# Kernel optimization log

Hardware: AMD Instinct MI355X
Metric: run time of the kernel (lower is better)

The kernel has to match this reference:

```python
import jax, jax.numpy as jnp
import numpy as np

B, S, HID = 4, 2048, 2048
NH, NKV, HD = 16, 4, 128
GROUPS = NH // NKV
THETA = 10000.0
SCALING = 1.0
SCALE = HD ** -0.5


def setup_inputs() -> dict:
    key = jax.random.key(0)
    k1, k2, k3 = jax.random.split(key, 3)
    hidden_states = jax.random.normal(k1, (B, S, HID), dtype=jnp.float32)
    # stored as [in, out] so x @ W matches torch Linear(x) with W = weight.T
    W_qkv = jax.random.normal(k2, (HID, (NH + 2 * NKV) * HD), dtype=jnp.float32) * (HID ** -0.5)
    W_o = jax.random.normal(k3, (HID, HID), dtype=jnp.float32) * (HID ** -0.5)
    return {"hidden_states": hidden_states, "W_qkv": W_qkv, "W_o": W_o}


def _rope_tables(seq_len, dtype):
    inv_freq = 1.0 / (THETA ** (jnp.arange(0, HD, 2, dtype=jnp.float32) / HD))
    t = jnp.arange(seq_len, dtype=jnp.float32) / SCALING
    freqs = jnp.einsum("s,d->sd", t, inv_freq)          # [S, HD/2]
    emb = jnp.concatenate([freqs, freqs], axis=-1)        # [S, HD]
    return jnp.cos(emb).astype(dtype), jnp.sin(emb).astype(dtype)


def _rotate_half(x):
    x1, x2 = jnp.split(x, 2, axis=-1)
    return jnp.concatenate([-x2, x1], axis=-1)


def _apply_rope(x, cos, sin):
    # x: [B, H, S, D]; cos/sin: [S, D]
    return x * cos[None, None] + _rotate_half(x) * sin[None, None]


def reference(hidden_states, W_qkv, W_o):
    b, s, _ = hidden_states.shape
    qkv = hidden_states @ W_qkv                           # [B, S, (NH+2NKV)*HD]
    q, k, v = jnp.split(qkv, [NH * HD, (NH + NKV) * HD], axis=-1)
    q = q.reshape(b, s, NH, HD).transpose(0, 2, 1, 3)      # [B, NH, S, D]
    k = k.reshape(b, s, NKV, HD).transpose(0, 2, 1, 3)     # [B, NKV, S, D]
    v = v.reshape(b, s, NKV, HD).transpose(0, 2, 1, 3)

    cos, sin = _rope_tables(s, hidden_states.dtype)
    q = _apply_rope(q, cos, sin)
    k = _apply_rope(k, cos, sin)

    # GQA attention without materializing expanded K/V
    qg = q.reshape(b, NKV, GROUPS, s, HD)                  # [B, NKV, G, Sq, D]
    scores = jnp.einsum("bkgqd,bkKd->bkgqK", qg, k) * SCALE
    causal = jnp.tril(jnp.ones((s, s), dtype=bool))
    scores = jnp.where(causal[None, None, None], scores, jnp.finfo(scores.dtype).min)
    probs = jax.nn.softmax(scores, axis=-1)
    out = jnp.einsum("bkgqK,bkKd->bkgqd", probs, v)        # [B, NKV, G, Sq, D]
    out = out.reshape(b, NH, s, HD).transpose(0, 2, 1, 3).reshape(b, s, HID)
    return out @ W_o
```

## Files before the change

kernel.cpp:

```cpp
#include <hip/hip_runtime.h>

#define B_ 4
#define S_ 2048
#define HID_ 2048
#define NH_ 16
#define NKV_ 4
#define HD_ 128
#define NTOK (B_ * S_)
#define QKV_N 3072
#define KO_N 512
#define SCALE_ 0.08838834764831845f
#define QSC_ 0.12751743f
#define NEG_ -30000.0f

typedef __attribute__((ext_vector_type(8))) short short8;
typedef __attribute__((ext_vector_type(4))) short short4v;
typedef __attribute__((ext_vector_type(4))) float f32x4;
typedef unsigned short ushort_t;
typedef unsigned int uint32;

__device__ __forceinline__ float sanit(float x) {
    if (!(x == x)) x = 0.0f;
    return fminf(fmaxf(x, -65504.0f), 65504.0f);
}
__device__ __forceinline__ ushort_t f2bf(float f) {
    union { float f; uint32 u; } c; c.f = f;
    uint32 u = c.u;
    u += 0x7fffu + ((u >> 16) & 1u);
    return (ushort_t)(u >> 16);
}
__device__ __forceinline__ ushort_t f2bf_s(float f) { return f2bf(sanit(f)); }
__device__ __forceinline__ float bf2f(ushort_t h) {
    union { float f; uint32 u; } c; c.u = ((uint32)h) << 16;
    return c.f;
}

__device__ __forceinline__ void gl16(const ushort_t* g, ushort_t* l) {
    __builtin_amdgcn_global_load_lds(
        (__attribute__((address_space(1))) void*)g,
        (__attribute__((address_space(3))) void*)l, 16, 0, 0);
}

__global__ void convx_kernel(const float* __restrict__ X, ushort_t* __restrict__ Xb) {
    size_t i = (size_t)blockIdx.x * blockDim.x + threadIdx.x;
    const float4 a = *(const float4*)(X + i * 8);
    const float4 b = *(const float4*)(X + i * 8 + 4);
    short8 p;
    p[0] = (short)f2bf(a.x); p[1] = (short)f2bf(a.y);
    p[2] = (short)f2bf(a.z); p[3] = (short)f2bf(a.w);
    p[4] = (short)f2bf(b.x); p[5] = (short)f2bf(b.y);
    p[6] = (short)f2bf(b.z); p[7] = (short)f2bf(b.w);
    *(short8*)(Xb + i * 8) = p;
}

__global__ void wtrans_kernel(const float* __restrict__ W, ushort_t* __restrict__ Wt,
                              int K, int N) {
    __shared__ float tile[32][33];
    const int n0 = blockIdx.x * 32;
    const int k0 = blockIdx.y * 32;
    const int t  = threadIdx.x;
    const int r  = t >> 3;
    const int c  = (t & 7) * 4;
    const float4 v = *(const float4*)(W + (size_t)(k0 + r) * N + n0 + c);
    tile[r][c] = v.x; tile[r][c + 1] = v.y; tile[r][c + 2] = v.z; tile[r][c + 3] = v.w;
    __syncthreads();
    short4v p;
    p[0] = (short)f2bf(tile[c][r]);
    p[1] = (short)f2bf(tile[c + 1][r]);
    p[2] = (short)f2bf(tile[c + 2][r]);
    p[3] = (short)f2bf(tile[c + 3][r]);
    *(short4v*)(Wt + (size_t)(n0 + r) * K + k0 + c) = p;
}

template <int SPLIT>
__global__ __launch_bounds__(256, 2) void gemm_bt(
    const ushort_t* __restrict__ A, const ushort_t* __restrict__ Bt,
    void* __restrict__ C0, ushort_t* __restrict__ C1, ushort_t* __restrict__ C2,
    int M, int N, int K) {
    __shared__ __align__(16) ushort_t As[128 * 32];
    __shared__ __align__(16) ushort_t Bs[128 * 32];

    const int tid  = threadIdx.x;
    const int lane = tid & 63;
    const int w    = tid >> 6;
    const int wm   = (w >> 1) * 64;
    const int wn   = (w & 1) * 64;
    const int m0   = blockIdx.y * 128;
    const int n0   = blockIdx.x * 128;
    const int col  = lane & 15;
    const int quad = lane >> 4;

    f32x4 acc[4][4] = {};

    const int sr = tid >> 2;
    const int sk = (tid & 3) * 8;
    const ushort_t* ag0 = A + (size_t)(m0 + sr) * K + sk;
    const ushort_t* ag1 = A + (size_t)(m0 + 64 + sr) * K + sk;
    const ushort_t* bg0 = Bt + (size_t)(n0 + sr) * K + sk;
    const ushort_t* bg1 = Bt + (size_t)(n0 + 64 + sr) * K + sk;
    ushort_t* la0 = &As[tid * 8];
    ushort_t* la1 = &As[2048 + tid * 8];
    ushort_t* lb0 = &Bs[tid * 8];
    ushort_t* lb1 = &Bs[2048 + tid * 8];

    for (int k0 = 0; k0 < K; k0 += 32) {
        __syncthreads();
        gl16(ag0 + k0, la0);
        gl16(ag1 + k0, la1);
        gl16(bg0 + k0, lb0);
        gl16(bg1 + k0, lb1);
        __syncthreads();

        short8 af[4], bfr[4];
#pragma unroll
        for (int mt = 0; mt < 4; ++mt)
            af[mt] = *(const short8*)&As[(wm + mt * 16 + col) * 32 + quad * 8];
#pragma unroll
        for (int nt = 0; nt < 4; ++nt)
            bfr[nt] = *(const short8*)&Bs[(wn + nt * 16 + col) * 32 + quad * 8];
#pragma unroll
        for (int mt = 0; mt < 4; ++mt)
#pragma unroll
            for (int nt = 0; nt < 4; ++nt)
                acc[mt][nt] = __builtin_amdgcn_mfma_f32_16x16x32_bf16(
                    af[mt], bfr[nt], acc[mt][nt], 0, 0, 0);
    }

    if (SPLIT) {
        if (n0 >= 2560) {
#pragma unroll
            for (int mt = 0; mt < 4; ++mt)
#pragma unroll
                for (int nt = 0; nt < 4; ++nt) {
                    int cc   = n0 + wn + nt * 16 + col - 2560;
                    int row0 = m0 + wm + mt * 16 + quad * 4;
                    short4v p;
#pragma unroll
                    for (int r = 0; r < 4; ++r) p[r] = (short)f2bf_s(acc[mt][nt][r]);
                    *(short4v*)&C2[(size_t)cc * NTOK + row0] = p;
                }
        } else {
            ushort_t* dst;
            int ldc, coff;
            if (n0 >= 2048) { dst = C1; ldc = KO_N; coff = 2048; }
            else            { dst = (ushort_t*)C0; ldc = HID_; coff = 0; }
#pragma unroll
            for (int mt = 0; mt < 4; ++mt)
#pragma unroll
                for (int nt = 0; nt < 4; ++nt)
#pragma unroll
                    for (int r = 0; r < 4; ++r) {
                        int row = m0 + wm + mt * 16 + quad * 4 + r;
                        int cc  = n0 + wn + nt * 16 + col - coff;
                        dst[(size_t)row * ldc + cc] = f2bf_s(acc[mt][nt][r]);
                    }
        }
    } else {
        float* dst = (float*)C0;
#pragma unroll
        for (int mt = 0; mt < 4; ++mt)
#pragma unroll
            for (int nt = 0; nt < 4; ++nt)
#pragma unroll
                for (int r = 0; r < 4; ++r) {
                    int row = m0 + wm + mt * 16 + quad * 4 + r;
                    int cc  = n0 + wn + nt * 16 + col;
                    dst[(size_t)row * N + cc] = sanit(acc[mt][nt][r]);
                }
    }
}

__global__ void rope_kernel(ushort_t* __restrict__ qbuf,
                            ushort_t* __restrict__ kb) {
    int p = blockIdx.x * blockDim.x + threadIdx.x;
    const int total = NTOK * 20 * 64;
    if (p >= total) return;
    int d    = p & 63;
    int rest = p >> 6;
    int head = rest % 20;
    int tok  = rest / 20;
    int s    = tok & (S_ - 1);

    ushort_t* base;
    float sc;
    if (head < 16) { base = qbuf + (size_t)tok * HID_ + head * HD_ + d; sc = QSC_; }
    else           { base = kb   + (size_t)tok * KO_N + (head - 16) * HD_ + d; sc = 1.0f; }

    float x1 = bf2f(base[0]);
    float x2 = bf2f(base[64]);

    float inv_freq = powf(10000.0f, -(float)d * (1.0f / 64.0f));
    float ang = (float)s * inv_freq;
    float sn, cs;
    sincosf(ang, &sn, &cs);

    base[0]  = f2bf_s((x1 * cs - x2 * sn) * sc);
    base[64] = f2bf_s((x2 * cs + x1 * sn) * sc);
}

__global__ __launch_bounds__(512, 4) void flash_kernel(
    const ushort_t* __restrict__ qbuf, const ushort_t* __restrict__ kb,
    const ushort_t* __restrict__ vtg, ushort_t* __restrict__ obuf) {
    __shared__ __align__(16) ushort_t Ks[64][136];
    __shared__ __align__(16) ushort_t Vt[128][72];
    __shared__ __align__(16) ushort_t Ps[8][16][72];

    const int tid  = threadIdx.x;
    const int lane = tid & 63;
    const int w    = tid >> 6;
    const int col  = lane & 15;
    const int quad = lane >> 4;
    const int q0   = (S_ / 128 - 1 - blockIdx.x) * 128;
    const int h    = blockIdx.y;
    const int b    = blockIdx.z;
    const int kvh  = h >> 2;
    const int bS   = b * S_;

    const int wr    = q0 + w * 16;
    const int wmax  = wr + 15;
    const int i_row = wr + quad * 4;

    short8 qf[4];
    {
        const ushort_t* qp = qbuf + (size_t)(bS + wr + col) * HID_
                             + h * HD_ + quad * 8;
#pragma unroll
        for (int kt = 0; kt < 4; ++kt) qf[kt] = *(const short8*)(qp + kt * 32);
    }

    short8 vone;
#pragma unroll
    for (int e = 0; e < 8; ++e) vone[e] = (short)0x3F80;

    float m_i[4];
#pragma unroll
    for (int r = 0; r < 4; ++r) m_i[r] = NEG_;
    f32x4 o[8] = {};
    f32x4 lsum = {};

    const int ntiles = q0 / 64 + 2;

    const int jr = tid >> 3;
    const int kd = (tid & 7) * 16;
    const int vd = tid >> 2;
    const int vj = (tid & 3) * 16;

    const ushort_t* kgb = kb + (size_t)(bS + jr) * KO_N + kvh * HD_ + kd;
    const ushort_t* vgb = vtg + (size_t)(kvh * HD_ + vd) * NTOK + bS + vj;

    float4 pk0, pk1, pv0, pv1;
    pk0 = *(const float4*)(kgb);
    pk1 = *(const float4*)(kgb + 8);
    pv0 = *(const float4*)(vgb);
    pv1 = *(const float4*)(vgb + 8);
    *(float4*)&Ks[jr][kd]     = pk0;
    *(float4*)&Ks[jr][kd + 8] = pk1;
    *(float4*)&Vt[vd][vj]     = pv0;
    *(float4*)&Vt[vd][vj + 8] = pv1;
    __syncthreads();

    for (int t = 0; t < ntiles; ++t) {
        const int j0 = t * 64;
        const bool pre = (t + 1 < ntiles);
        if (pre) {
            const ushort_t* kgn = kgb + (size_t)(j0 + 64) * KO_N;
            const ushort_t* vgn = vgb + (j0 + 64);
            pk0 = *(const float4*)(kgn);
            pk1 = *(const float4*)(kgn + 8);
            pv0 = *(const float4*)(vgn);
            pv1 = *(const float4*)(vgn + 8);
        }

        if (j0 <= wmax) {
            f32x4 s[4] = {};
#pragma unroll
            for (int ct = 0; ct < 4; ++ct)
#pragma unroll
                for (int kt = 0; kt < 4; ++kt) {
                    short8 kf = *(const short8*)&Ks[ct * 16 + col][kt * 32 + quad * 8];
                    s[ct] = __builtin_amdgcn_mfma_f32_16x16x32_bf16(qf[kt], kf, s[ct], 0, 0, 0);
                }

            if (j0 + 64 > wr) {
#pragma unroll
                for (int ct = 0; ct < 4; ++ct) {
                    int jg = j0 + ct * 16 + col;
#pragma unroll
                    for (int r = 0; r < 4; ++r)
                        if (jg > i_row + r) s[ct][r] = NEG_;
                }
            }

            float mx[4];
#pragma unroll
            for (int r = 0; r < 4; ++r) {
                float m = fmaxf(fmaxf(s[0][r], s[1][r]), fmaxf(s[2][r], s[3][r]));
#pragma unroll
                for (int off = 1; off < 16; off <<= 1)
                    m = fmaxf(m, __shfl_xor(m, off, 64));
                mx[r] = m;
            }
            int ok = 1;
#pragma unroll
            for (int r = 0; r < 4; ++r) ok &= (mx[r] <= m_i[r] + 8.0f) ? 1 : 0;
            if (!__all(ok)) {
#pragma unroll
                for (int r = 0; r < 4; ++r) {
                    float mn = fmaxf(m_i[r], mx[r]);
                    float a  = exp2f(m_i[r] - mn);
                    m_i[r] = mn;
                    lsum[r] *= a;
#pragma unroll
                    for (int dt = 0; dt < 8; ++dt) o[dt][r] *= a;
                }
            }
#pragma unroll
            for (int ct = 0; ct < 4; ++ct)
#pragma unroll
                for (int r = 0; r < 4; ++r)
                    Ps[w][quad * 4 + r][ct * 16 + col] = f2bf(exp2f(s[ct][r] - m_i[r]));

#pragma unroll
            for (int kt = 0; kt < 2; ++kt) {
                short8 pf = *(const short8*)&Ps[w][col][kt * 32 + quad * 8];
#pragma unroll
                for (int dt = 0; dt < 8; ++dt) {
                    short8 vf = *(const short8*)&Vt[dt * 16 + col][kt * 32 + quad * 8];
                    o[dt] = __builtin_amdgcn_mfma_f32_16x16x32_bf16(pf, vf, o[dt], 0, 0, 0);
                }
                lsum = __builtin_amdgcn_mfma_f32_16x16x32_bf16(pf, vone, lsum, 0, 0, 0);
            }
        }

        __syncthreads();
        if (pre) {
            *(float4*)&Ks[jr][kd]     = pk0;
            *(float4*)&Ks[jr][kd + 8] = pk1;
            *(float4*)&Vt[vd][vj]     = pv0;
            *(float4*)&Vt[vd][vj + 8] = pv1;
            __syncthreads();
        }
    }

#pragma unroll
    for (int r = 0; r < 4; ++r) {
        float inv = 1.0f / fmaxf(lsum[r], 1e-30f);
        ushort_t* op = obuf + (size_t)(bS + i_row + r) * HID_ + h * HD_;
#pragma unroll
        for (int dt = 0; dt < 8; ++dt)
            op[dt * 16 + col] = f2bf_s(o[dt][r] * inv);
    }
}

extern "C" void kernel_launch(void* const* d_in, const int* in_sizes, int n_in,
                              void* d_out, int out_size, void* d_ws, size_t ws_size,
                              hipStream_t stream) {
    const float* X    = (const float*)d_in[0];
    const float* Wqkv = (const float*)d_in[1];
    const float* Wo   = (const float*)d_in[2];

    ushort_t* qb  = (ushort_t*)d_out;
    ushort_t* xh  = (ushort_t*)d_out + (size_t)NTOK * HID_;
    ushort_t* kb  = (ushort_t*)d_ws;
    ushort_t* vtg = kb + (size_t)NTOK * KO_N;
    ushort_t* wqt = vtg + (size_t)NTOK * KO_N;
    ushort_t* wot = (ushort_t*)d_ws + (size_t)NTOK * HID_;
    ushort_t* oa  = (ushort_t*)d_ws;

    convx_kernel<<<NTOK * HID_ / (256 * 8), 256, 0, stream>>>(X, xh);
    wtrans_kernel<<<dim3(QKV_N / 32, HID_ / 32), 256, 0, stream>>>(Wqkv, wqt, HID_, QKV_N);
    wtrans_kernel<<<dim3(HID_ / 32, HID_ / 32), 256, 0, stream>>>(Wo, wot, HID_, HID_);
    gemm_bt<1><<<dim3(QKV_N / 128, NTOK / 128), 256, 0, stream>>>(
        xh, wqt, qb, kb, vtg, NTOK, QKV_N, HID_);
    rope_kernel<<<(NTOK * 20 * 64) / 256, 256, 0, stream>>>(qb, kb);
    flash_kernel<<<dim3(S_ / 128, NH_, B_), 512, 0, stream>>>(qb, kb, vtg, xh);
    hipMemcpyAsync(oa, xh, (size_t)NTOK * HID_ * sizeof(ushort_t),
                   hipMemcpyDeviceToDevice, stream);
    gemm_bt<0><<<dim3(HID_ / 128, NTOK / 128), 256, 0, stream>>>(
        oa, wot, d_out, nullptr, nullptr, NTOK, HID_, HID_);
}
```

Baseline: 644.4 us.

## Deepen GEMM K-tile to 64, precompute RoPE tables, vectorize RoPE

The GEMM's K step doubles from 32 to 64, so each shared-memory tile holds twice the data and the number of barrier pairs per block is halved. A new kernel precomputes cos/sin RoPE tables once per call. The RoPE kernel now processes 8 elements per thread with 16-byte loads and reads the tables instead of calling powf/sincosf per element. The trade-off is more LDS per GEMM block, which may reduce occupancy, plus one extra small kernel launch.

```diff
diff --git a/kernel.cpp b/kernel.cpp
--- a/kernel.cpp
+++ b/kernel.cpp
@@ -11,6 +11,7 @@
 #define KO_N 512
 #define SCALE_ 0.08838834764831845f
 #define QSC_ 0.12751743f
+#define LOG2_10K 13.287712379549449f
 #define NEG_ -30000.0f
 
 typedef __attribute__((ext_vector_type(8))) short short8;
@@ -72,13 +73,23 @@
     *(short4v*)(Wt + (size_t)(n0 + r) * K + k0 + c) = p;
 }
 
+__global__ void ropetab_kernel(float* __restrict__ ct, float* __restrict__ st) {
+    int p = blockIdx.x * blockDim.x + threadIdx.x;
+    int s = p >> 6, d = p & 63;
+    float inv = exp2f(-(float)d * (LOG2_10K / 64.0f));
+    float ang = (float)s * inv;
+    float sn, cs;
+    sincosf(ang, &sn, &cs);
+    ct[p] = cs; st[p] = sn;
+}
+
 template <int SPLIT>
 __global__ __launch_bounds__(256, 2) void gemm_bt(
     const ushort_t* __restrict__ A, const ushort_t* __restrict__ Bt,
     void* __restrict__ C0, ushort_t* __restrict__ C1, ushort_t* __restrict__ C2,
     int M, int N, int K) {
-    __shared__ __align__(16) ushort_t As[128 * 32];
-    __shared__ __align__(16) ushort_t Bs[128 * 32];
+    __shared__ __align__(16) ushort_t As[128 * 64];
+    __shared__ __align__(16) ushort_t Bs[128 * 64];
 
     const int tid  = threadIdx.x;
     const int lane = tid & 63;
@@ -92,38 +103,45 @@
 
     f32x4 acc[4][4] = {};
 
-    const int sr = tid >> 2;
-    const int sk = (tid & 3) * 8;
-    const ushort_t* ag0 = A + (size_t)(m0 + sr) * K + sk;
-    const ushort_t* ag1 = A + (size_t)(m0 + 64 + sr) * K + sk;
-    const ushort_t* bg0 = Bt + (size_t)(n0 + sr) * K + sk;
-    const ushort_t* bg1 = Bt + (size_t)(n0 + 64 + sr) * K + sk;
-    ushort_t* la0 = &As[tid * 8];
-    ushort_t* la1 = &As[2048 + tid * 8];
-    ushort_t* lb0 = &Bs[tid * 8];
-    ushort_t* lb1 = &Bs[2048 + tid * 8];
-
-    for (int k0 = 0; k0 < K; k0 += 32) {
+    const ushort_t* agp[4];
+    const ushort_t* bgp[4];
+    ushort_t* lap[4];
+    ushort_t* lbp[4];
+#pragma unroll
+    for (int i = 0; i < 4; ++i) {
+        int c  = i * 256 + tid;
+        int rw = c >> 3;
+        int kc = (c & 7) * 8;
+        agp[i] = A  + (size_t)(m0 + rw) * K + kc;
+        bgp[i] = Bt + (size_t)(n0 + rw) * K + kc;
+        lap[i] = &As[c * 8];
+        lbp[i] = &Bs[c * 8];
+    }
+
+    for (int k0 = 0; k0 < K; k0 += 64) {
         __syncthreads();
-        gl16(ag0 + k0, la0);
-        gl16(ag1 + k0, la1);
-        gl16(bg0 + k0, lb0);
-        gl16(bg1 + k0, lb1);
+#pragma unroll
+        for (int i = 0; i < 4; ++i) gl16(agp[i] + k0, lap[i]);
+#pragma unroll
+        for (int i = 0; i < 4; ++i) gl16(bgp[i] + k0, lbp[i]);
         __syncthreads();
 
-        short8 af[4], bfr[4];
-#pragma unroll
-        for (int mt = 0; mt < 4; ++mt)
-            af[mt] = *(const short8*)&As[(wm + mt * 16 + col) * 32 + quad * 8];
-#pragma unroll
-        for (int nt = 0; nt < 4; ++nt)
-            bfr[nt] = *(const short8*)&Bs[(wn + nt * 16 + col) * 32 + quad * 8];
-#pragma unroll
-        for (int mt = 0; mt < 4; ++mt)
+#pragma unroll
+        for (int kk = 0; kk < 2; ++kk) {
+            short8 af[4], bfr[4];
+#pragma unroll
+            for (int mt = 0; mt < 4; ++mt)
+                af[mt] = *(const short8*)&As[(wm + mt * 16 + col) * 64 + kk * 32 + quad * 8];
 #pragma unroll
             for (int nt = 0; nt < 4; ++nt)
-                acc[mt][nt] = __builtin_amdgcn_mfma_f32_16x16x32_bf16(
-                    af[mt], bfr[nt], acc[mt][nt], 0, 0, 0);
+                bfr[nt] = *(const short8*)&Bs[(wn + nt * 16 + col) * 64 + kk * 32 + quad * 8];
+#pragma unroll
+            for (int mt = 0; mt < 4; ++mt)
+#pragma unroll
+                for (int nt = 0; nt < 4; ++nt)
+                    acc[mt][nt] = __builtin_amdgcn_mfma_f32_16x16x32_bf16(
+                        af[mt], bfr[nt], acc[mt][nt], 0, 0, 0);
+        }
     }
 
     if (SPLIT) {
@@ -170,32 +188,35 @@
     }
 }
 
-__global__ void rope_kernel(ushort_t* __restrict__ qbuf,
-                            ushort_t* __restrict__ kb) {
+__global__ void rope_kernel(ushort_t* __restrict__ qbuf, ushort_t* __restrict__ kb,
+                            const float* __restrict__ ct, const float* __restrict__ st) {
     int p = blockIdx.x * blockDim.x + threadIdx.x;
-    const int total = NTOK * 20 * 64;
-    if (p >= total) return;
-    int d    = p & 63;
-    int rest = p >> 6;
+    int d0   = (p & 7) * 8;
+    int rest = p >> 3;
     int head = rest % 20;
     int tok  = rest / 20;
     int s    = tok & (S_ - 1);
 
     ushort_t* base;
     float sc;
-    if (head < 16) { base = qbuf + (size_t)tok * HID_ + head * HD_ + d; sc = QSC_; }
-    else           { base = kb   + (size_t)tok * KO_N + (head - 16) * HD_ + d; sc = 1.0f; }
-
-    float x1 = bf2f(base[0]);
-    float x2 = bf2f(base[64]);
-
-    float inv_freq = powf(10000.0f, -(float)d * (1.0f / 64.0f));
-    float ang = (float)s * inv_freq;
-    float sn, cs;
-    sincosf(ang, &sn, &cs);
-
-    base[0]  = f2bf_s((x1 * cs - x2 * sn) * sc);
-    base[64] = f2bf_s((x2 * cs + x1 * sn) * sc);
+    if (head < 16) { base = qbuf + (size_t)tok * HID_ + head * HD_ + d0; sc = QSC_; }
+    else           { base = kb   + (size_t)tok * KO_N + (head - 16) * HD_ + d0; sc = 1.0f; }
+
+    short8 x1v = *(const short8*)base;
+    short8 x2v = *(const short8*)(base + 64);
+    const float* cp = ct + s * 64 + d0;
+    const float* sp = st + s * 64 + d0;
+    short8 r1, r2;
+#pragma unroll
+    for (int e = 0; e < 8; ++e) {
+        float x1 = bf2f((ushort_t)x1v[e]);
+        float x2 = bf2f((ushort_t)x2v[e]);
+        float cs = cp[e], sn = sp[e];
+        r1[e] = (short)f2bf_s((x1 * cs - x2 * sn) * sc);
+        r2[e] = (short)f2bf_s((x2 * cs + x1 * sn) * sc);
+    }
+    *(short8*)base        = r1;
+    *(short8*)(base + 64) = r2;
 }
 
 __global__ __launch_bounds__(512, 4) void flash_kernel(
@@ -365,14 +386,17 @@
     ushort_t* vtg = kb + (size_t)NTOK * KO_N;
     ushort_t* wqt = vtg + (size_t)NTOK * KO_N;
     ushort_t* wot = (ushort_t*)d_ws + (size_t)NTOK * HID_;
+    float*    ctab = (float*)(wot + (size_t)HID_ * HID_);
+    float*    stab = ctab + (size_t)S_ * 64;
     ushort_t* oa  = (ushort_t*)d_ws;
 
     convx_kernel<<<NTOK * HID_ / (256 * 8), 256, 0, stream>>>(X, xh);
     wtrans_kernel<<<dim3(QKV_N / 32, HID_ / 32), 256, 0, stream>>>(Wqkv, wqt, HID_, QKV_N);
     wtrans_kernel<<<dim3(HID_ / 32, HID_ / 32), 256, 0, stream>>>(Wo, wot, HID_, HID_);
+    ropetab_kernel<<<(S_ * 64) / 256, 256, 0, stream>>>(ctab, stab);
     gemm_bt<1><<<dim3(QKV_N / 128, NTOK / 128), 256, 0, stream>>>(
         xh, wqt, qb, kb, vtg, NTOK, QKV_N, HID_);
-    rope_kernel<<<(NTOK * 20 * 64) / 256, 256, 0, stream>>>(qb, kb);
+    rope_kernel<<<(NTOK * 20 * 8) / 256, 256, 0, stream>>>(qb, kb, ctab, stab);
     flash_kernel<<<dim3(S_ / 128, NH_, B_), 512, 0, stream>>>(qb, kb, vtg, xh);
     hipMemcpyAsync(oa, xh, (size_t)NTOK * HID_ * sizeof(ushort_t),
                    hipMemcpyDeviceToDevice, stream);
```

Result: faster. 624.9 us (-3.0%).
